# Kernel optimization log

Measured on AMD Instinct MI355X. Metric: run time of the kernel, lower is better.

## Reference

```python
import jax, jax.numpy as jnp
import numpy as np

HIDDEN = 2048
HEAD = 256
VDIM = 512  # double_v_dim=True -> 2*head_size
GAMMA = 0.96875
SCALE_BASE = 512.0  # xpos default


def _rotate_every_two(x):
    # (x0, x1, x2, x3, ...) -> (-x1, x0, -x3, x2, ...)
    x1 = x[..., ::2]
    x2 = x[..., 1::2]
    return jnp.stack((-x2, x1), axis=-1).reshape(x.shape)


def _xpos(x, downscale=False, offset=0):
    # Standard XPOS (rotary + exponential scaling) as used in RetNet repos.
    S, d = x.shape[1], x.shape[2]
    d2 = d // 2
    scale_vec = (jnp.arange(0, d, 2, dtype=jnp.float32) + 0.4 * d) / (1.4 * d)  # [d2]
    pos = jnp.arange(S + offset, dtype=jnp.float32)
    scale = scale_vec[None, :] ** (pos[:, None] / SCALE_BASE)  # [S+off, d2]
    inv_freq = 1.0 / (10000.0 ** (jnp.arange(d2, dtype=jnp.float32) / d2))
    sinusoid = pos[:, None] * inv_freq[None, :]  # [S+off, d2]
    sin, cos = jnp.sin(sinusoid), jnp.cos(sinusoid)
    scale, sin, cos = scale[-S:], sin[-S:], cos[-S:]
    if downscale:
        scale = 1.0 / scale
    sin_s = jnp.repeat(sin * scale, 2, axis=-1)  # duplicate_interleave -> [S, d]
    cos_s = jnp.repeat(cos * scale, 2, axis=-1)
    return x * cos_s[None] + _rotate_every_two(x) * sin_s[None]


def _decay_matrix(S):
    # D[n, m] = gamma^(n-m) for n >= m else 0 (NaN/overflow-safe)
    n = jnp.arange(S, dtype=jnp.float32)
    diff = n[:, None] - n[None, :]
    mask = diff >= 0
    return jnp.where(mask, GAMMA ** jnp.where(mask, diff, 0.0), 0.0)


def setup_inputs() -> dict:
    key = jax.random.key(0)
    k1, k2, k3, k4 = jax.random.split(key, 4)
    B, S = 4, 4096
    X = jax.random.normal(k1, (B, S, HIDDEN), dtype=jnp.float32)
    W_Q = jax.random.normal(k2, (HIDDEN, HEAD), dtype=jnp.float32) / HIDDEN
    W_K = jax.random.normal(k3, (HIDDEN, HEAD), dtype=jnp.float32) / HIDDEN
    W_V = jax.random.normal(k4, (HIDDEN, VDIM), dtype=jnp.float32) / HIDDEN
    return {"X": X, "W_Q": W_Q, "W_K": W_K, "W_V": W_V}


def reference(X, W_Q, W_K, W_V):
    S = X.shape[1]
    Q = _xpos(X @ W_Q)                      # [B, S, HEAD]
    K = _xpos(X @ W_K, downscale=True)      # [B, S, HEAD]
    V = X @ W_V                             # [B, S, VDIM]
    D = _decay_matrix(S)                    # [S, S]
    retention = jnp.einsum('bqd,bkd->bqk', Q, K) * D[None]  # [B, S, S]
    return retention @ V                    # [B, S, VDIM]
```

## Files before the change

### kernel.cpp

```cpp
#include <hip/hip_runtime.h>
#include <math.h>

#define NB 4
#define SEQ 4096
#define HID 2048
#define DH 256
#define DV 512
#define CHUNK 128
#define NCH 32
#define MROWS (NB * SEQ)
#define GAMMA 0.96875f
#define GAMMA_INV 1.0322580645161290f
#define LOG2_GAMMA (-0.045803689613124794f)
#define LOG2_10000 13.287712379549449f

typedef __attribute__((ext_vector_type(8))) short short8;
typedef __attribute__((ext_vector_type(4))) float floatx4;

__device__ __forceinline__ unsigned short bf16_rne(float v) {
    unsigned int u = __float_as_uint(v);
    u += 0x7fff + ((u >> 16) & 1);
    return (unsigned short)(u >> 16);
}
__device__ __forceinline__ float b2f(unsigned short h) {
    return __uint_as_float((unsigned int)h << 16);
}

__device__ __forceinline__ void gld16(const void* g, void* l) {
    __builtin_amdgcn_global_load_lds(
        reinterpret_cast<const __attribute__((address_space(1))) unsigned int*>(
            reinterpret_cast<uintptr_t>(g)),
        reinterpret_cast<__attribute__((address_space(3))) unsigned int*>(
            reinterpret_cast<uintptr_t>(l)),
        16, 0, 0);
}

__global__ __launch_bounds__(256) void xcvt_kernel(
    const float* __restrict__ X, unsigned short* __restrict__ Xb)
{
    const int i = blockIdx.x * 256 + threadIdx.x;
    float4 x = ((const float4*)X)[i];
    ushort4 h;
    h.x = bf16_rne(x.x); h.y = bf16_rne(x.y);
    h.z = bf16_rne(x.z); h.w = bf16_rne(x.w);
    ((ushort4*)Xb)[i] = h;
}

__global__ __launch_bounds__(256) void wcvt_kernel(
    const float* __restrict__ WQ, const float* __restrict__ WK,
    const float* __restrict__ WV, unsigned short* __restrict__ Bt)
{
    __shared__ unsigned short sh[64][65];
    const int bid = blockIdx.x;
    const int kt = bid & 31;
    const int ntile = bid >> 5;
    const int k0 = kt * 64, n0 = ntile * 64;

    const float* W; int ld, nl0;
    if (n0 < 256)      { W = WQ; ld = DH; nl0 = n0; }
    else if (n0 < 512) { W = WK; ld = DH; nl0 = n0 - 256; }
    else               { W = WV; ld = DV; nl0 = n0 - 512; }

    const int t = threadIdx.x;
#pragma unroll
    for (int p = 0; p < 4; p++) {
        const int kl = (t >> 4) + p * 16;
        const int ng = (t & 15) * 4;
        float4 w = *(const float4*)&W[(size_t)(k0 + kl) * ld + nl0 + ng];
        sh[kl][ng + 0] = bf16_rne(w.x);
        sh[kl][ng + 1] = bf16_rne(w.y);
        sh[kl][ng + 2] = bf16_rne(w.z);
        sh[kl][ng + 3] = bf16_rne(w.w);
    }
    __syncthreads();
#pragma unroll
    for (int p = 0; p < 4; p++) {
        const int nl = (t >> 4) + p * 16;
        const int kg = (t & 15) * 4;
        ushort4 h;
        h.x = sh[kg + 0][nl]; h.y = sh[kg + 1][nl];
        h.z = sh[kg + 2][nl]; h.w = sh[kg + 3][nl];
        *(ushort4*)&Bt[(size_t)(n0 + nl) * HID + k0 + kg] = h;
    }
}

__global__ __launch_bounds__(512, 2) void qkv_mfma_kernel(
    const unsigned short* __restrict__ Xb, const unsigned short* __restrict__ Bt,
    unsigned short* __restrict__ Qb, unsigned short* __restrict__ Kb,
    unsigned short* __restrict__ Kt, unsigned short* __restrict__ Vt)
{
    __shared__ unsigned short lds[2 * 32768];

    const int bid = blockIdx.x;
    const int xcd = bid & 7;
    const int idx = bid >> 3;
    const int mt  = (xcd << 3) | (idx >> 2);
    const int nt  = idx & 3;
    const int m0 = mt * 256, n0 = nt * 256;

    const int t = threadIdx.x;
    const int w = t >> 6, lane = t & 63;
    const int wr = w >> 2;
    const int wc = w & 3;

    floatx4 acc[8][4];
#pragma unroll
    for (int i = 0; i < 8; i++)
#pragma unroll
        for (int j = 0; j < 4; j++) acc[i][j] = (floatx4)0.0f;

    const int rl = lane >> 3;
    const int sg = (lane & 7) ^ rl;

    const int fr = lane & 15, g = lane >> 4;
    const int x7 = fr & 7;
    const int soff0 = ((g ^ x7) << 3);
    const int soff1 = (((4 | g) ^ x7) << 3);

#define STAGE_HT(isB, h, dbuf, kt)                                            \
    {                                                                         \
        const unsigned short* gsrc =                                          \
            ((isB) ? Bt + (size_t)(n0 + (h) * 128 + w * 16 + rl) * HID        \
                   : Xb + (size_t)(m0 + (h) * 128 + w * 16 + rl) * HID)       \
            + (size_t)(kt) * 64 + sg * 8;                                     \
        unsigned short* ldst = &lds[(dbuf) * 32768 + ((isB) ? 16384 : 0)      \
                                    + ((h) * 128 + w * 16) * 64];             \
        gld16(gsrc, ldst);                                                    \
        gld16(gsrc + (size_t)8 * HID, ldst + 8 * 64);                         \
    }

#define READ_A(ih)                                                            \
    _Pragma("unroll")                                                         \
    for (int i2 = 0; i2 < 4; i2++) {                                          \
        const int row = wr * 128 + ((ih) * 4 + i2) * 16 + fr;                 \
        ah[i2][0] = *(const short8*)&lds[cb + row * 64 + soff0];              \
        ah[i2][1] = *(const short8*)&lds[cb + row * 64 + soff1];              \
    }

#define READ_B(jh)                                                            \
    _Pragma("unroll")                                                         \
    for (int j2 = 0; j2 < 2; j2++) {                                          \
        const int row = wc * 64 + ((jh) * 2 + j2) * 16 + fr;                  \
        bh[(jh) * 2 + j2][0] = *(const short8*)&lds[cb + 16384 + row * 64 + soff0]; \
        bh[(jh) * 2 + j2][1] = *(const short8*)&lds[cb + 16384 + row * 64 + soff1]; \
    }

#define MFMA16(ib, jb)                                                        \
    _Pragma("unroll")                                                         \
    for (int i2 = 0; i2 < 4; i2++)                                            \
        _Pragma("unroll")                                                     \
        for (int j2 = 0; j2 < 2; j2++) {                                      \
            acc[(ib) + i2][(jb) + j2] = __builtin_amdgcn_mfma_f32_16x16x32_bf16( \
                ah[i2][0], bh[(jb) + j2][0], acc[(ib) + i2][(jb) + j2], 0, 0, 0); \
            acc[(ib) + i2][(jb) + j2] = __builtin_amdgcn_mfma_f32_16x16x32_bf16( \
                ah[i2][1], bh[(jb) + j2][1], acc[(ib) + i2][(jb) + j2], 0, 0, 0); \
        }

    STAGE_HT(0, 0, 0, 0); STAGE_HT(0, 1, 0, 0);
    STAGE_HT(1, 0, 0, 0); STAGE_HT(1, 1, 0, 0);
    asm volatile("s_waitcnt vmcnt(0)" ::: "memory");
    __builtin_amdgcn_s_barrier();
    __builtin_amdgcn_sched_barrier(0);

    int cur = 0;
    for (int kt = 0; kt < 32; ++kt) {
        const int nxt = cur ^ 1;
        if (kt + 1 < 32) {
            STAGE_HT(0, 0, nxt, kt + 1); STAGE_HT(0, 1, nxt, kt + 1);
            STAGE_HT(1, 0, nxt, kt + 1); STAGE_HT(1, 1, nxt, kt + 1);
        }
        const int cb = cur * 32768;
        short8 ah[4][2], bh[4][2];

        READ_A(0); READ_B(0);
        __builtin_amdgcn_s_barrier();
        __builtin_amdgcn_sched_barrier(0);
        __builtin_amdgcn_s_setprio(1);
        MFMA16(0, 0);
        __builtin_amdgcn_s_setprio(0);
        __builtin_amdgcn_s_barrier();
        __builtin_amdgcn_sched_barrier(0);

        READ_B(1);
        __builtin_amdgcn_s_barrier();
        __builtin_amdgcn_sched_barrier(0);
        __builtin_amdgcn_s_setprio(1);
        MFMA16(0, 2);
        __builtin_amdgcn_s_setprio(0);
        __builtin_amdgcn_s_barrier();
        __builtin_amdgcn_sched_barrier(0);

        READ_A(1);
        __builtin_amdgcn_s_barrier();
        __builtin_amdgcn_sched_barrier(0);
        __builtin_amdgcn_s_setprio(1);
        MFMA16(4, 0);
        __builtin_amdgcn_s_setprio(0);
        __builtin_amdgcn_s_barrier();
        __builtin_amdgcn_sched_barrier(0);

        __builtin_amdgcn_s_setprio(1);
        MFMA16(4, 2);
        __builtin_amdgcn_s_setprio(0);
        asm volatile("s_waitcnt vmcnt(0)" ::: "memory");
        __builtin_amdgcn_s_barrier();
        __builtin_amdgcn_sched_barrier(0);
        cur = nxt;
    }
#undef STAGE_HT
#undef READ_A
#undef READ_B
#undef MFMA16

    const int cl = lane & 15, rq = (lane >> 4) << 2;
    if (n0 >= 512) {
#pragma unroll
        for (int i = 0; i < 8; i++)
#pragma unroll
            for (int j = 0; j < 4; j++) {
                const int c = n0 - 512 + wc * 64 + j * 16 + cl;
#pragma unroll
                for (int r = 0; r < 4; r++) {
                    const int m = m0 + wr * 128 + i * 16 + rq + r;
                    Vt[(size_t)c * MROWS + m] = bf16_rne(acc[i][j][r]);
                }
            }
    } else {
        const bool isQ = (n0 < 256);
        unsigned short* dst = isQ ? Qb : Kb;
        const float sgn = isQ ? 1.f : -1.f;
#pragma unroll
        for (int j = 0; j < 4; j++) {
            const int c = wc * 64 + j * 16 + cl;
            const float jj = (float)(c >> 1);
            const float sv = (2.f * jj + 0.4f * 256.f) * (1.f / (1.4f * 256.f));
            const float l2sv = __log2f(sv) * sgn * (1.f / 512.f);
            const float invf = exp2f(jj * (-LOG2_10000 / 128.f));
            const bool odd = (c & 1) != 0;
#pragma unroll
            for (int i = 0; i < 8; i++) {
#pragma unroll
                for (int r = 0; r < 4; r++) {
                    const int m = m0 + wr * 128 + i * 16 + rq + r;
                    const float s = (float)(m & (SEQ - 1));
                    const float x = acc[i][j][r];
                    const float p = __shfl_xor(x, 1, 64);
                    const float sc = exp2f(s * l2sv);
                    const float ang = s * invf;
                    const float sn = __sinf(ang), cs = __cosf(ang);
                    const float o = odd ? sc * (x * cs + p * sn)
                                        : sc * (x * cs - p * sn);
                    const unsigned short hv = bf16_rne(o);
                    dst[(size_t)m * DH + c] = hv;
                    if (!isQ) Kt[(size_t)c * MROWS + m] = hv;
                }
            }
        }
    }
}

__global__ __launch_bounds__(512, 2) void chunk_kv_kernel(
    const unsigned short* __restrict__ Kt, const unsigned short* __restrict__ Vt,
    float* __restrict__ Ut)
{
    __shared__ unsigned short As[128 * 128];
    __shared__ unsigned short Bs[128 * 128];

    const int bid = blockIdx.x;
    const int dht = bid & 1;
    const int vq  = (bid >> 1) & 3;
    const int c   = (bid >> 3) & 31;
    const int b   = bid >> 8;
    const int dh0 = dht * 128, dv0 = vq * 128;
    const int row0 = b * SEQ + c * CHUNK;

    const int t = threadIdx.x;
    const int w = t >> 6, lane = t & 63;
    const int wm = (w & 1) << 6;
    const int wn = (w >> 1) << 5;
    const int fr = lane & 15, g = lane >> 4;

    floatx4 acc[4][2];
#pragma unroll
    for (int i = 0; i < 4; i++)
#pragma unroll
        for (int j = 0; j < 2; j++) acc[i][j] = (floatx4)0.0f;

    {
        const int ar = lane >> 4, asl = lane & 15;
#pragma unroll
        for (int q = 0; q < 4; q++) {
            const int row = w * 16 + q * 4 + ar;
            const int ssl = asl ^ (row & 15);
            gld16(&Vt[(size_t)(dv0 + row) * MROWS + row0 + ssl * 8],
                  &As[(w * 16 + q * 4) * 128]);
        }
    }
    {
        const int kr = t >> 2, kc4 = t & 3;
#pragma unroll
        for (int p = 0; p < 4; p++) {
            const int col = kc4 * 8 + p * 32;
            const unsigned short* src = &Kt[(size_t)(dh0 + kr) * MROWS + row0 + col];
            ushort4 k0v = *(const ushort4*)src;
            ushort4 k1v = *(const ushort4*)(src + 4);
            float gsc = exp2f((float)(CHUNK - col) * LOG2_GAMMA);
            ushort4 h0, h1;
            h0.x = bf16_rne(b2f(k0v.x) * gsc); gsc *= GAMMA_INV;
            h0.y = bf16_rne(b2f(k0v.y) * gsc); gsc *= GAMMA_INV;
            h0.z = bf16_rne(b2f(k0v.z) * gsc); gsc *= GAMMA_INV;
            h0.w = bf16_rne(b2f(k0v.w) * gsc); gsc *= GAMMA_INV;
            h1.x = bf16_rne(b2f(k1v.x) * gsc); gsc *= GAMMA_INV;
            h1.y = bf16_rne(b2f(k1v.y) * gsc); gsc *= GAMMA_INV;
            h1.z = bf16_rne(b2f(k1v.z) * gsc); gsc *= GAMMA_INV;
            h1.w = bf16_rne(b2f(k1v.w) * gsc);
            const int wsl = (kc4 + p * 4) ^ (kr & 15);
            *(ushort4*)&Bs[kr * 128 + wsl * 8] = h0;
            *(ushort4*)&Bs[kr * 128 + wsl * 8 + 4] = h1;
        }
    }
    __syncthreads();

#pragma nounroll
    for (int s = 0; s < 4; s++) {
        short8 a[4], bb[2];
#pragma unroll
        for (int i = 0; i < 4; i++)
            a[i] = *(const short8*)&As[(wm + i * 16 + fr) * 128
                                       + (((s * 4 + g) ^ fr) << 3)];
#pragma unroll
        for (int j = 0; j < 2; j++)
            bb[j] = *(const short8*)&Bs[(wn + j * 16 + fr) * 128
                                        + (((s * 4 + g) ^ fr) << 3)];
#pragma unroll
        for (int i = 0; i < 4; i++)
#pragma unroll
            for (int j = 0; j < 2; j++)
                acc[i][j] = __builtin_amdgcn_mfma_f32_16x16x32_bf16(a[i], bb[j], acc[i][j], 0, 0, 0);
    }

    const int cl = lane & 15, rq = (lane >> 4) << 2;
    const size_t ubase = ((size_t)(b * NCH + c) * DV + dv0) * DH + dh0;
#pragma unroll
    for (int i = 0; i < 4; i++)
#pragma unroll
        for (int j = 0; j < 2; j++) {
            const int n = wn + j * 16 + cl;
#pragma unroll
            for (int r = 0; r < 4; r++) {
                const int m = wm + i * 16 + rq + r;
                Ut[ubase + (size_t)m * DH + n] = acc[i][j][r];
            }
        }
}

__global__ __launch_bounds__(256) void scan_kernel(
    const float* __restrict__ Ut, unsigned short* __restrict__ Sb)
{
    const int t = blockIdx.x * 256 + threadIdx.x;
    const int b = t >> 17;
    const int r = t & 131071;
    const float gC = exp2f((float)CHUNK * LOG2_GAMMA);
    float s = 0.f;
    const size_t base = (size_t)b * NCH * 131072 + r;
    for (int c = 0; c < NCH; c++) {
        const size_t off = base + (size_t)c * 131072;
        const float u = Ut[off];
        Sb[off] = bf16_rne(s);
        s = gC * s + u;
    }
}

__global__ __launch_bounds__(512, 1) void out_mfma_kernel(
    const unsigned short* __restrict__ Qb, const unsigned short* __restrict__ Kb,
    const unsigned short* __restrict__ Vt, const unsigned short* __restrict__ Sb,
    float* __restrict__ out)
{
    __shared__ unsigned short Pa[128 * 136];
    __shared__ unsigned short As[128 * 64];
    __shared__ unsigned short Bs[128 * 64];

    const int bid = blockIdx.x;
    const int vq = bid & 3;
    const int c  = (bid >> 2) & 31;
    const int b  = bid >> 7;
    const int dv0 = vq * 128;
    const int row0 = b * SEQ + c * CHUNK;

    const int t = threadIdx.x;
    const int w = t >> 6, lane = t & 63;
    const int wm = (w & 1) << 6;
    const int wn = (w >> 1) << 5;
    const int fr = lane & 15, g = lane >> 4, fq = g * 8;
    const int cl = lane & 15, rq = (lane >> 4) << 2;
    const int rl8 = lane >> 3, sl8 = lane & 7;
    const int ssl8 = sl8 ^ rl8;
    const int x7 = fr & 7;

    floatx4 acc[4][2];
#pragma unroll
    for (int i = 0; i < 4; i++)
#pragma unroll
        for (int j = 0; j < 2; j++) acc[i][j] = (floatx4)0.0f;

    for (int d0 = 0; d0 < DH; d0 += 64) {
        __syncthreads();
#pragma unroll
        for (int q = 0; q < 2; q++) {
            const int row = w * 16 + q * 8 + rl8;
            gld16(&Qb[(size_t)(row0 + row) * DH + d0 + ssl8 * 8],
                  &As[(w * 16 + q * 8) * 64]);
            gld16(&Kb[(size_t)(row0 + row) * DH + d0 + ssl8 * 8],
                  &Bs[(w * 16 + q * 8) * 64]);
        }
        __syncthreads();
#pragma nounroll
        for (int s = 0; s < 2; s++) {
            short8 a[4], bb[2];
#pragma unroll
            for (int i = 0; i < 4; i++)
                a[i] = *(const short8*)&As[(wm + i * 16 + fr) * 64
                                           + (((s * 4 + g) ^ x7) << 3)];
#pragma unroll
            for (int j = 0; j < 2; j++)
                bb[j] = *(const short8*)&Bs[(wn + j * 16 + fr) * 64
                                            + (((s * 4 + g) ^ x7) << 3)];
#pragma unroll
            for (int i = 0; i < 4; i++)
#pragma unroll
                for (int j = 0; j < 2; j++)
                    acc[i][j] = __builtin_amdgcn_mfma_f32_16x16x32_bf16(a[i], bb[j], acc[i][j], 0, 0, 0);
        }
    }

#pragma unroll
    for (int i = 0; i < 4; i++)
#pragma unroll
        for (int j = 0; j < 2; j++) {
            const int jj = wn + j * 16 + cl;
#pragma unroll
            for (int r = 0; r < 4; r++) {
                const int ii = wm + i * 16 + rq + r;
                const int diff = ii - jj;
                const float v = (diff >= 0) ? acc[i][j][r] * exp2f((float)diff * LOG2_GAMMA) : 0.f;
                Pa[ii * 136 + jj] = bf16_rne(v);
            }
            acc[i][j] = (floatx4)0.0f;
        }

    for (int k0 = 0; k0 < CHUNK; k0 += 64) {
        __syncthreads();
#pragma unroll
        for (int q = 0; q < 2; q++) {
            const int row = w * 16 + q * 8 + rl8;
            gld16(&Vt[(size_t)(dv0 + row) * MROWS + row0 + k0 + ssl8 * 8],
                  &Bs[(w * 16 + q * 8) * 64]);
        }
        __syncthreads();
#pragma nounroll
        for (int s = 0; s < 2; s++) {
            short8 a[4], bb[2];
#pragma unroll
            for (int i = 0; i < 4; i++)
                a[i] = *(const short8*)&Pa[(wm + i * 16 + fr) * 136 + k0 + s * 32 + fq];
#pragma unroll
            for (int j = 0; j < 2; j++)
                bb[j] = *(const short8*)&Bs[(wn + j * 16 + fr) * 64
                                            + (((s * 4 + g) ^ x7) << 3)];
#pragma unroll
            for (int i = 0; i < 4; i++)
#pragma unroll
                for (int j = 0; j < 2; j++)
                    acc[i][j] = __builtin_amdgcn_mfma_f32_16x16x32_bf16(a[i], bb[j], acc[i][j], 0, 0, 0);
        }
    }

    const size_t sbbase = ((size_t)(b * NCH + c) * DV + dv0) * DH;
    const int xr = t >> 2, xc4 = t & 3;
    const float gx = exp2f((float)xr * LOG2_GAMMA);
    for (int d0 = 0; d0 < DH; d0 += 64) {
        __syncthreads();
#pragma unroll
        for (int s = 0; s < 2; s++) {
            const int col = s * 32 + xc4 * 8;
            const unsigned short* src = &Qb[(size_t)(row0 + xr) * DH + d0 + col];
            ushort4 q0 = *(const ushort4*)src;
            ushort4 q1 = *(const ushort4*)(src + 4);
            ushort4 h0, h1;
            h0.x = bf16_rne(b2f(q0.x) * gx); h0.y = bf16_rne(b2f(q0.y) * gx);
            h0.z = bf16_rne(b2f(q0.z) * gx); h0.w = bf16_rne(b2f(q0.w) * gx);
            h1.x = bf16_rne(b2f(q1.x) * gx); h1.y = bf16_rne(b2f(q1.y) * gx);
            h1.z = bf16_rne(b2f(q1.z) * gx); h1.w = bf16_rne(b2f(q1.w) * gx);
            const int wsl = (s * 4 + xc4) ^ (xr & 7);
            *(ushort4*)&As[xr * 64 + wsl * 8] = h0;
            *(ushort4*)&As[xr * 64 + wsl * 8 + 4] = h1;
        }
#pragma unroll
        for (int q = 0; q < 2; q++) {
            const int row = w * 16 + q * 8 + rl8;
            gld16(&Sb[sbbase + (size_t)row * DH + d0 + ssl8 * 8],
                  &Bs[(w * 16 + q * 8) * 64]);
        }
        __syncthreads();
#pragma nounroll
        for (int s = 0; s < 2; s++) {
            short8 a[4], bb[2];
#pragma unroll
            for (int i = 0; i < 4; i++)
                a[i] = *(const short8*)&As[(wm + i * 16 + fr) * 64
                                           + (((s * 4 + g) ^ x7) << 3)];
#pragma unroll
            for (int j = 0; j < 2; j++)
                bb[j] = *(const short8*)&Bs[(wn + j * 16 + fr) * 64
                                            + (((s * 4 + g) ^ x7) << 3)];
#pragma unroll
            for (int i = 0; i < 4; i++)
#pragma unroll
                for (int j = 0; j < 2; j++)
                    acc[i][j] = __builtin_amdgcn_mfma_f32_16x16x32_bf16(a[i], bb[j], acc[i][j], 0, 0, 0);
        }
    }

#pragma unroll
    for (int i = 0; i < 4; i++)
#pragma unroll
        for (int j = 0; j < 2; j++) {
            const int dv = dv0 + wn + j * 16 + cl;
#pragma unroll
            for (int r = 0; r < 4; r++) {
                const int m = row0 + wm + i * 16 + rq + r;
                out[(size_t)m * DV + dv] = acc[i][j][r];
            }
        }
}

extern "C" void kernel_launch(void* const* d_in, const int* in_sizes, int n_in,
                              void* d_out, int out_size, void* d_ws, size_t ws_size,
                              hipStream_t stream) {
    const float* X  = (const float*)d_in[0];
    const float* WQ = (const float*)d_in[1];
    const float* WK = (const float*)d_in[2];
    const float* WV = (const float*)d_in[3];
    float* out = (float*)d_out;

    char* ws = (char*)d_ws;
    unsigned short* Qb = (unsigned short*)ws;
    unsigned short* Kb = Qb + (size_t)MROWS * DH;
    unsigned short* Kt = Kb + (size_t)MROWS * DH;
    unsigned short* Vt = Kt + (size_t)MROWS * DH;
    unsigned short* Sb = Vt + (size_t)MROWS * DV;
    float*          Ut = (float*)(Sb + (size_t)NB * NCH * DV * DH);
    unsigned short* Xb = (unsigned short*)Ut;
    unsigned short* Bt = (unsigned short*)(Ut + (size_t)NB * NCH * DV * DH);

    xcvt_kernel<<<(MROWS * HID / 4) / 256, 256, 0, stream>>>(X, Xb);
    wcvt_kernel<<<512, 256, 0, stream>>>(WQ, WK, WV, Bt);
    qkv_mfma_kernel<<<256, 512, 0, stream>>>(Xb, Bt, Qb, Kb, Kt, Vt);
    chunk_kv_kernel<<<1024, 512, 0, stream>>>(Kt, Vt, Ut);
    scan_kernel<<<2048, 256, 0, stream>>>(Ut, Sb);
    out_mfma_kernel<<<512, 512, 0, stream>>>(Qb, Kb, Vt, Sb, out);
}
```

Measured before the change: 363.6 us.

## Interleave per-half-tile global loads into the MFMA phases of the projection GEMM

New measurement: 356.6 us. Within noise of the previous version (-1.9%).

```diff
diff --git a/kernel.cpp b/kernel.cpp
--- a/kernel.cpp
+++ b/kernel.cpp
@@ -117,12 +117,12 @@
     const int soff0 = ((g ^ x7) << 3);
     const int soff1 = (((4 | g) ^ x7) << 3);
 
-#define STAGE_HT(isB, h, dbuf, kt)                                            \
+#define STAGE_HT(isB, h, dbuf, ktile)                                         \
     {                                                                         \
         const unsigned short* gsrc =                                          \
             ((isB) ? Bt + (size_t)(n0 + (h) * 128 + w * 16 + rl) * HID        \
                    : Xb + (size_t)(m0 + (h) * 128 + w * 16 + rl) * HID)       \
-            + (size_t)(kt) * 64 + sg * 8;                                     \
+            + (size_t)(ktile) * 64 + sg * 8;                                  \
         unsigned short* ldst = &lds[(dbuf) * 32768 + ((isB) ? 16384 : 0)      \
                                     + ((h) * 128 + w * 16) * 64];             \
         gld16(gsrc, ldst);                                                    \
@@ -156,61 +156,73 @@
                 ah[i2][1], bh[(jb) + j2][1], acc[(ib) + i2][(jb) + j2], 0, 0, 0); \
         }
 
+#define BAR_SB()  { __builtin_amdgcn_s_barrier(); __builtin_amdgcn_sched_barrier(0); }
+
     STAGE_HT(0, 0, 0, 0); STAGE_HT(0, 1, 0, 0);
     STAGE_HT(1, 0, 0, 0); STAGE_HT(1, 1, 0, 0);
-    asm volatile("s_waitcnt vmcnt(0)" ::: "memory");
-    __builtin_amdgcn_s_barrier();
-    __builtin_amdgcn_sched_barrier(0);
-
-    int cur = 0;
-    for (int kt = 0; kt < 32; ++kt) {
-        const int nxt = cur ^ 1;
-        if (kt + 1 < 32) {
-            STAGE_HT(0, 0, nxt, kt + 1); STAGE_HT(0, 1, nxt, kt + 1);
-            STAGE_HT(1, 0, nxt, kt + 1); STAGE_HT(1, 1, nxt, kt + 1);
-        }
-        const int cb = cur * 32768;
+    STAGE_HT(1, 0, 1, 1); STAGE_HT(1, 1, 1, 1);
+    asm volatile("s_waitcnt vmcnt(4)" ::: "memory");
+    BAR_SB();
+
+    for (int kt = 0; kt < 32; kt += 2) {
         short8 ah[4][2], bh[4][2];
-
-        READ_A(0); READ_B(0);
-        __builtin_amdgcn_s_barrier();
-        __builtin_amdgcn_sched_barrier(0);
-        __builtin_amdgcn_s_setprio(1);
-        MFMA16(0, 0);
-        __builtin_amdgcn_s_setprio(0);
-        __builtin_amdgcn_s_barrier();
-        __builtin_amdgcn_sched_barrier(0);
-
-        READ_B(1);
-        __builtin_amdgcn_s_barrier();
-        __builtin_amdgcn_sched_barrier(0);
-        __builtin_amdgcn_s_setprio(1);
-        MFMA16(0, 2);
-        __builtin_amdgcn_s_setprio(0);
-        __builtin_amdgcn_s_barrier();
-        __builtin_amdgcn_sched_barrier(0);
-
-        READ_A(1);
-        __builtin_amdgcn_s_barrier();
-        __builtin_amdgcn_sched_barrier(0);
-        __builtin_amdgcn_s_setprio(1);
-        MFMA16(4, 0);
-        __builtin_amdgcn_s_setprio(0);
-        __builtin_amdgcn_s_barrier();
-        __builtin_amdgcn_sched_barrier(0);
-
-        __builtin_amdgcn_s_setprio(1);
-        MFMA16(4, 2);
-        __builtin_amdgcn_s_setprio(0);
-        asm volatile("s_waitcnt vmcnt(0)" ::: "memory");
-        __builtin_amdgcn_s_barrier();
-        __builtin_amdgcn_sched_barrier(0);
-        cur = nxt;
+        {
+            const int cb = 0;
+            READ_A(0); READ_B(0);
+            STAGE_HT(0, 0, 1, kt + 1);
+            BAR_SB();
+            __builtin_amdgcn_s_setprio(1); MFMA16(0, 0); __builtin_amdgcn_s_setprio(0);
+            BAR_SB();
+            READ_B(1);
+            STAGE_HT(0, 1, 1, kt + 1);
+            BAR_SB();
+            __builtin_amdgcn_s_setprio(1); MFMA16(0, 2); __builtin_amdgcn_s_setprio(0);
+            BAR_SB();
+            READ_A(1);
+            if (kt + 2 < 32) STAGE_HT(1, 0, 0, kt + 2);
+            BAR_SB();
+            __builtin_amdgcn_s_setprio(1); MFMA16(4, 0); __builtin_amdgcn_s_setprio(0);
+            BAR_SB();
+            if (kt + 2 < 32) {
+                STAGE_HT(1, 1, 0, kt + 2);
+                asm volatile("s_waitcnt vmcnt(4)" ::: "memory");
+            } else {
+                asm volatile("s_waitcnt vmcnt(0)" ::: "memory");
+            }
+            BAR_SB();
+            __builtin_amdgcn_s_setprio(1); MFMA16(4, 2); __builtin_amdgcn_s_setprio(0);
+            BAR_SB();
+        }
+        {
+            const int cb = 32768;
+            READ_A(0); READ_B(0);
+            if (kt + 2 < 32) STAGE_HT(0, 0, 0, kt + 2);
+            BAR_SB();
+            __builtin_amdgcn_s_setprio(1); MFMA16(0, 0); __builtin_amdgcn_s_setprio(0);
+            BAR_SB();
+            READ_B(1);
+            if (kt + 2 < 32) STAGE_HT(0, 1, 0, kt + 2);
+            BAR_SB();
+            __builtin_amdgcn_s_setprio(1); MFMA16(0, 2); __builtin_amdgcn_s_setprio(0);
+            BAR_SB();
+            READ_A(1);
+            if (kt + 3 < 32) STAGE_HT(1, 0, 1, kt + 3);
+            BAR_SB();
+            __builtin_amdgcn_s_setprio(1); MFMA16(4, 0); __builtin_amdgcn_s_setprio(0);
+            BAR_SB();
+            if (kt + 3 < 32) STAGE_HT(1, 1, 1, kt + 3);
+            if (kt + 2 < 32)
+                asm volatile("s_waitcnt vmcnt(4)" ::: "memory");
+            BAR_SB();
+            __builtin_amdgcn_s_setprio(1); MFMA16(4, 2); __builtin_amdgcn_s_setprio(0);
+            BAR_SB();
+        }
     }
 #undef STAGE_HT
 #undef READ_A
 #undef READ_B
 #undef MFMA16
+#undef BAR_SB
 
     const int cl = lane & 15, rq = (lane >> 4) << 2;
     if (n0 >= 512) {
```

## Shrink QKV GEMM tiles to 128x128 with simple single-buffered loop

Applied to the files above, without the earlier changes.

Result: no change. 364.0 us (+0.1%).

```diff
diff --git a/kernel.cpp b/kernel.cpp
--- a/kernel.cpp
+++ b/kernel.cpp
@@ -84,144 +84,79 @@
     }
 }
 
-__global__ __launch_bounds__(512, 2) void qkv_mfma_kernel(
+__global__ __launch_bounds__(256, 4) void qkv_mfma_kernel(
     const unsigned short* __restrict__ Xb, const unsigned short* __restrict__ Bt,
     unsigned short* __restrict__ Qb, unsigned short* __restrict__ Kb,
     unsigned short* __restrict__ Kt, unsigned short* __restrict__ Vt)
 {
-    __shared__ unsigned short lds[2 * 32768];
+    __shared__ unsigned short As[128 * 64];
+    __shared__ unsigned short Bs[128 * 64];
 
     const int bid = blockIdx.x;
     const int xcd = bid & 7;
-    const int idx = bid >> 3;
-    const int mt  = (xcd << 3) | (idx >> 2);
-    const int nt  = idx & 3;
-    const int m0 = mt * 256, n0 = nt * 256;
+    const int nt  = (bid >> 3) & 7;
+    const int mt  = (xcd << 4) | (bid >> 6);
+    const int m0 = mt * 128, n0 = nt * 128;
 
     const int t = threadIdx.x;
     const int w = t >> 6, lane = t & 63;
-    const int wr = w >> 2;
-    const int wc = w & 3;
-
-    floatx4 acc[8][4];
-#pragma unroll
-    for (int i = 0; i < 8; i++)
+    const int wm = (w & 1) << 6;
+    const int wn = (w >> 1) << 6;
+
+    floatx4 acc[4][4];
+#pragma unroll
+    for (int i = 0; i < 4; i++)
 #pragma unroll
         for (int j = 0; j < 4; j++) acc[i][j] = (floatx4)0.0f;
 
     const int rl = lane >> 3;
     const int sg = (lane & 7) ^ rl;
+    const unsigned short* const gA = Xb + (size_t)(m0 + w * 32 + rl) * HID + sg * 8;
+    const unsigned short* const gB = Bt + (size_t)(n0 + w * 32 + rl) * HID + sg * 8;
 
     const int fr = lane & 15, g = lane >> 4;
     const int x7 = fr & 7;
     const int soff0 = ((g ^ x7) << 3);
     const int soff1 = (((4 | g) ^ x7) << 3);
 
-#define STAGE_HT(isB, h, dbuf, kt)                                            \
-    {                                                                         \
-        const unsigned short* gsrc =                                          \
-            ((isB) ? Bt + (size_t)(n0 + (h) * 128 + w * 16 + rl) * HID        \
-                   : Xb + (size_t)(m0 + (h) * 128 + w * 16 + rl) * HID)       \
-            + (size_t)(kt) * 64 + sg * 8;                                     \
-        unsigned short* ldst = &lds[(dbuf) * 32768 + ((isB) ? 16384 : 0)      \
-                                    + ((h) * 128 + w * 16) * 64];             \
-        gld16(gsrc, ldst);                                                    \
-        gld16(gsrc + (size_t)8 * HID, ldst + 8 * 64);                         \
-    }
-
-#define READ_A(ih)                                                            \
-    _Pragma("unroll")                                                         \
-    for (int i2 = 0; i2 < 4; i2++) {                                          \
-        const int row = wr * 128 + ((ih) * 4 + i2) * 16 + fr;                 \
-        ah[i2][0] = *(const short8*)&lds[cb + row * 64 + soff0];              \
-        ah[i2][1] = *(const short8*)&lds[cb + row * 64 + soff1];              \
-    }
-
-#define READ_B(jh)                                                            \
-    _Pragma("unroll")                                                         \
-    for (int j2 = 0; j2 < 2; j2++) {                                          \
-        const int row = wc * 64 + ((jh) * 2 + j2) * 16 + fr;                  \
-        bh[(jh) * 2 + j2][0] = *(const short8*)&lds[cb + 16384 + row * 64 + soff0]; \
-        bh[(jh) * 2 + j2][1] = *(const short8*)&lds[cb + 16384 + row * 64 + soff1]; \
-    }
-
-#define MFMA16(ib, jb)                                                        \
-    _Pragma("unroll")                                                         \
-    for (int i2 = 0; i2 < 4; i2++)                                            \
-        _Pragma("unroll")                                                     \
-        for (int j2 = 0; j2 < 2; j2++) {                                      \
-            acc[(ib) + i2][(jb) + j2] = __builtin_amdgcn_mfma_f32_16x16x32_bf16( \
-                ah[i2][0], bh[(jb) + j2][0], acc[(ib) + i2][(jb) + j2], 0, 0, 0); \
-            acc[(ib) + i2][(jb) + j2] = __builtin_amdgcn_mfma_f32_16x16x32_bf16( \
-                ah[i2][1], bh[(jb) + j2][1], acc[(ib) + i2][(jb) + j2], 0, 0, 0); \
-        }
-
-    STAGE_HT(0, 0, 0, 0); STAGE_HT(0, 1, 0, 0);
-    STAGE_HT(1, 0, 0, 0); STAGE_HT(1, 1, 0, 0);
-    asm volatile("s_waitcnt vmcnt(0)" ::: "memory");
-    __builtin_amdgcn_s_barrier();
-    __builtin_amdgcn_sched_barrier(0);
-
-    int cur = 0;
-    for (int kt = 0; kt < 32; ++kt) {
-        const int nxt = cur ^ 1;
-        if (kt + 1 < 32) {
-            STAGE_HT(0, 0, nxt, kt + 1); STAGE_HT(0, 1, nxt, kt + 1);
-            STAGE_HT(1, 0, nxt, kt + 1); STAGE_HT(1, 1, nxt, kt + 1);
-        }
-        const int cb = cur * 32768;
-        short8 ah[4][2], bh[4][2];
-
-        READ_A(0); READ_B(0);
-        __builtin_amdgcn_s_barrier();
-        __builtin_amdgcn_sched_barrier(0);
-        __builtin_amdgcn_s_setprio(1);
-        MFMA16(0, 0);
-        __builtin_amdgcn_s_setprio(0);
-        __builtin_amdgcn_s_barrier();
-        __builtin_amdgcn_sched_barrier(0);
-
-        READ_B(1);
-        __builtin_amdgcn_s_barrier();
-        __builtin_amdgcn_sched_barrier(0);
-        __builtin_amdgcn_s_setprio(1);
-        MFMA16(0, 2);
-        __builtin_amdgcn_s_setprio(0);
-        __builtin_amdgcn_s_barrier();
-        __builtin_amdgcn_sched_barrier(0);
-
-        READ_A(1);
-        __builtin_amdgcn_s_barrier();
-        __builtin_amdgcn_sched_barrier(0);
-        __builtin_amdgcn_s_setprio(1);
-        MFMA16(4, 0);
-        __builtin_amdgcn_s_setprio(0);
-        __builtin_amdgcn_s_barrier();
-        __builtin_amdgcn_sched_barrier(0);
-
-        __builtin_amdgcn_s_setprio(1);
-        MFMA16(4, 2);
-        __builtin_amdgcn_s_setprio(0);
-        asm volatile("s_waitcnt vmcnt(0)" ::: "memory");
-        __builtin_amdgcn_s_barrier();
-        __builtin_amdgcn_sched_barrier(0);
-        cur = nxt;
-    }
-#undef STAGE_HT
-#undef READ_A
-#undef READ_B
-#undef MFMA16
+    for (int k0 = 0; k0 < HID; k0 += 64) {
+        __syncthreads();
+#pragma unroll
+        for (int q = 0; q < 4; q++) {
+            gld16(gA + (size_t)q * 8 * HID + k0, &As[(w * 32 + q * 8) * 64]);
+            gld16(gB + (size_t)q * 8 * HID + k0, &Bs[(w * 32 + q * 8) * 64]);
+        }
+        __syncthreads();
+
+#pragma nounroll
+        for (int s = 0; s < 2; s++) {
+            const int soff = s ? soff1 : soff0;
+            short8 ah[4], bh[4];
+#pragma unroll
+            for (int i = 0; i < 4; i++)
+                ah[i] = *(const short8*)&As[(wm + i * 16 + fr) * 64 + soff];
+#pragma unroll
+            for (int j = 0; j < 4; j++)
+                bh[j] = *(const short8*)&Bs[(wn + j * 16 + fr) * 64 + soff];
+#pragma unroll
+            for (int i = 0; i < 4; i++)
+#pragma unroll
+                for (int j = 0; j < 4; j++)
+                    acc[i][j] = __builtin_amdgcn_mfma_f32_16x16x32_bf16(
+                        ah[i], bh[j], acc[i][j], 0, 0, 0);
+        }
+    }
 
     const int cl = lane & 15, rq = (lane >> 4) << 2;
     if (n0 >= 512) {
 #pragma unroll
-        for (int i = 0; i < 8; i++)
+        for (int i = 0; i < 4; i++)
 #pragma unroll
             for (int j = 0; j < 4; j++) {
-                const int c = n0 - 512 + wc * 64 + j * 16 + cl;
+                const int c = n0 - 512 + wn + j * 16 + cl;
 #pragma unroll
                 for (int r = 0; r < 4; r++) {
-                    const int m = m0 + wr * 128 + i * 16 + rq + r;
+                    const int m = m0 + wm + i * 16 + rq + r;
                     Vt[(size_t)c * MROWS + m] = bf16_rne(acc[i][j][r]);
                 }
             }
@@ -229,19 +164,20 @@
         const bool isQ = (n0 < 256);
         unsigned short* dst = isQ ? Qb : Kb;
         const float sgn = isQ ? 1.f : -1.f;
+        const int nb = isQ ? n0 : n0 - 256;
 #pragma unroll
         for (int j = 0; j < 4; j++) {
-            const int c = wc * 64 + j * 16 + cl;
+            const int c = nb + wn + j * 16 + cl;
             const float jj = (float)(c >> 1);
             const float sv = (2.f * jj + 0.4f * 256.f) * (1.f / (1.4f * 256.f));
             const float l2sv = __log2f(sv) * sgn * (1.f / 512.f);
             const float invf = exp2f(jj * (-LOG2_10000 / 128.f));
             const bool odd = (c & 1) != 0;
 #pragma unroll
-            for (int i = 0; i < 8; i++) {
+            for (int i = 0; i < 4; i++) {
 #pragma unroll
                 for (int r = 0; r < 4; r++) {
-                    const int m = m0 + wr * 128 + i * 16 + rq + r;
+                    const int m = m0 + wm + i * 16 + rq + r;
                     const float s = (float)(m & (SEQ - 1));
                     const float x = acc[i][j][r];
                     const float p = __shfl_xor(x, 1, 64);
@@ -555,7 +491,7 @@
 
     xcvt_kernel<<<(MROWS * HID / 4) / 256, 256, 0, stream>>>(X, Xb);
     wcvt_kernel<<<512, 256, 0, stream>>>(WQ, WK, WV, Bt);
-    qkv_mfma_kernel<<<256, 512, 0, stream>>>(Xb, Bt, Qb, Kb, Kt, Vt);
+    qkv_mfma_kernel<<<1024, 256, 0, stream>>>(Xb, Bt, Qb, Kb, Kt, Vt);
     chunk_kv_kernel<<<1024, 512, 0, stream>>>(Kt, Vt, Ut);
     scan_kernel<<<2048, 256, 0, stream>>>(Ut, Sb);
     out_mfma_kernel<<<512, 512, 0, stream>>>(Qb, Kb, Vt, Sb, out);
```
